# Kernel tuning notes

Hardware: AMD Instinct MI355X
Metric: run time of the kernel (lower is better)

The kernel has to match this reference:

```python
import jax, jax.numpy as jnp
import numpy as np

# SAWB clip coefficients (statistics-aware weight binning): alpha = C1*sqrt(E[w^2]) + C2*E[|w|]
SAWB_C1 = 12.68
SAWB_C2 = -12.80
Q_LEVELS = 127.0  # symmetric 8-bit


def sawb_quantize_sparse(W, mask):
    """Quantize only the nonzero (masked) weight values per-tensor, SAWB clip.
    Returns dequantized sparse weight (zeros stay zero), matching the
    original module which stores nnz values + indices and quantizes the
    nnz value vector."""
    m = mask.astype(W.dtype)
    n = jnp.maximum(jnp.sum(m), 1.0)
    m1 = jnp.sum(jnp.abs(W) * m) / n          # E[|w|] over nonzeros
    m2 = jnp.sum((W * W) * m) / n             # E[w^2] over nonzeros
    alpha = SAWB_C1 * jnp.sqrt(m2) + SAWB_C2 * m1
    scale = alpha / Q_LEVELS
    q = jnp.round(jnp.clip(W / scale, -Q_LEVELS, Q_LEVELS))
    return (q * scale) * m


def setup_inputs() -> dict:
    key = jax.random.key(0)
    k1, k2, k3, k4 = jax.random.split(key, 4)
    B, IC, H, Wsp = 16, 64, 224, 224
    OC, K = 64, 3
    x = jax.random.normal(k1, (B, IC, H, Wsp), dtype=jnp.float32)
    W = jax.random.normal(k2, (OC, IC, K, K), dtype=jnp.float32) * 0.05
    mask = jax.random.uniform(k3, (OC, IC, K, K)) > 0.9
    bias = jax.random.normal(k4, (OC,), dtype=jnp.float32) * 0.01
    return {"x": x, "W": W, "mask": mask, "bias": bias}


def reference(x, W, mask, bias):
    # Dequantized sparse weight (equivalent math to gather-based sparse
    # quantized conv kernel with fused dequant)
    Wq = sawb_quantize_sparse(W, mask)
    y = jax.lax.conv_general_dilated(
        x, Wq,
        window_strides=(1, 1),
        padding=((1, 1), (1, 1)),
        dimension_numbers=("NCHW", "OIHW", "NCHW"),
    )
    return y + bias[None, :, None, None]
```

## Files before the change

### kernel.cpp

```cpp
#include <hip/hip_runtime.h>
#include <hip/hip_bf16.h>
#include <math.h>

typedef __bf16 bfx8 __attribute__((ext_vector_type(8)));
typedef float f32x4 __attribute__((ext_vector_type(4)));

#define NELEM_W 36864
#define CHW     50176

__device__ __forceinline__ int detect_mask_kind(const void* mask, int tid, int nthreads,
                                                int* s_flags, int* s_kind) {
  if (tid < 8) s_flags[tid] = 0;
  __syncthreads();
  const unsigned int* mw = (const unsigned int*)mask;
  int lowbf = 0, notf32 = 0, anyf32 = 0, noti32 = 0, anyi1 = 0;
  for (int i = tid; i < 1024; i += nthreads) {
    unsigned v = mw[i];
    if ((v & 0xFFFFu) == 0x3F80u) lowbf = 1;
    if (!(v == 0u || v == 0x3F800000u)) notf32 = 1;
    if (v == 0x3F800000u) anyf32 = 1;
    if (!(v == 0u || v == 1u)) noti32 = 1;
    if (v == 1u) anyi1 = 1;
  }
  if (lowbf)  atomicOr(&s_flags[0], 1);
  if (notf32) atomicOr(&s_flags[1], 1);
  if (anyf32) atomicOr(&s_flags[2], 1);
  if (noti32) atomicOr(&s_flags[3], 1);
  if (anyi1)  atomicOr(&s_flags[4], 1);
  __syncthreads();
  if (tid == 0) {
    int kind;
    if (s_flags[0]) kind = 3;
    else if (!s_flags[1] && s_flags[2]) kind = 2;
    else if (!s_flags[3] && s_flags[4]) kind = 1;
    else kind = 0;
    *s_kind = kind;
  }
  __syncthreads();
  return *s_kind;
}

__device__ __forceinline__ bool mask_val(const void* mask, int kind, int e) {
  switch (kind) {
    case 1:  return ((const int*)mask)[e] != 0;
    case 2:  return ((const float*)mask)[e] != 0.0f;
    case 3:  return ((const unsigned short*)mask)[e] != 0;
    default: return ((const unsigned char*)mask)[e] != 0;
  }
}

__global__ __launch_bounds__(512) void stats_kernel(const float* __restrict__ W,
                                                    const void* __restrict__ mask,
                                                    float* __restrict__ ws_part) {
  __shared__ int s_flags[8]; __shared__ int s_kind;
  __shared__ float s_red[3][8];
  const int tid = threadIdx.x;
  int kind = detect_mask_kind(mask, tid, 512, s_flags, &s_kind);
  int e = blockIdx.x * 512 + tid;
  float w = W[e];
  bool m = mask_val(mask, kind, e);
  float s1 = m ? fabsf(w) : 0.f;
  float s2 = m ? w * w   : 0.f;
  float c  = m ? 1.f     : 0.f;
  #pragma unroll
  for (int o = 32; o > 0; o >>= 1) {
    s1 += __shfl_down(s1, o); s2 += __shfl_down(s2, o); c += __shfl_down(c, o);
  }
  int wv = tid >> 6;
  if ((tid & 63) == 0) { s_red[0][wv] = s1; s_red[1][wv] = s2; s_red[2][wv] = c; }
  __syncthreads();
  if (tid == 0) {
    float a = 0, b = 0, cc = 0;
    for (int i = 0; i < 8; i++) { a += s_red[0][i]; b += s_red[1][i]; cc += s_red[2][i]; }
    ws_part[blockIdx.x * 4 + 0] = a;
    ws_part[blockIdx.x * 4 + 1] = b;
    ws_part[blockIdx.x * 4 + 2] = cc;
  }
}

__global__ __launch_bounds__(512) void quant_kernel(const float* __restrict__ W,
                                                    const void* __restrict__ mask,
                                                    const float* __restrict__ ws_part,
                                                    float* __restrict__ ws_scale,
                                                    unsigned short* __restrict__ Bq) {
  __shared__ int s_flags[8]; __shared__ int s_kind;
  __shared__ float s_scale;
  const int tid = threadIdx.x;
  int kind = detect_mask_kind(mask, tid, 512, s_flags, &s_kind);
  if (tid == 0) {
    float a = 0, b = 0, cc = 0;
    for (int i = 0; i < 72; i++) { a += ws_part[i*4]; b += ws_part[i*4+1]; cc += ws_part[i*4+2]; }
    float n  = fmaxf(cc, 1.f);
    float m1 = a / n, m2 = b / n;
    float alpha = 12.68f * sqrtf(m2) - 12.80f * m1;
    float scale = alpha / 127.0f;
    s_scale = scale;
    if (blockIdx.x == 0) ws_scale[0] = scale;
  }
  __syncthreads();
  float scale = s_scale;
  int e = blockIdx.x * 512 + tid;
  float w = W[e];
  float q = 0.f;
  if (mask_val(mask, kind, e)) {
    float v = w / scale;
    v = fminf(fmaxf(v, -127.f), 127.f);
    q = rintf(v);
  }
  int kxy = e % 9; int t = e / 9; int ic = t & 63; int oc = t >> 6;
  __bf16 qb = (__bf16)q;
  Bq[(kxy * 64 + oc) * 64 + ic] = *(unsigned short*)&qb;
}

template<int NMF>
__device__ __forceinline__ void mfma_compute(const unsigned char* __restrict__ smem,
    const unsigned short* __restrict__ Bq, const float* __restrict__ ws_scale,
    const float* __restrict__ bias, float* __restrict__ out,
    int b, int y0, int x0, int wrow, int oc0, int mf0, int l15, int lg)
{
  f32x4 acc[NMF][2];
  #pragma unroll
  for (int m = 0; m < NMF; m++) { acc[m][0] = {0.f,0.f,0.f,0.f}; acc[m][1] = {0.f,0.f,0.f,0.f}; }

  #pragma unroll
  for (int ky = 0; ky < 3; ky++) {
    const int lrow = wrow + ky;
    #pragma unroll
    for (int kx = 0; kx < 3; kx++) {
      #pragma unroll
      for (int icb = 0; icb < 2; icb++) {
        const int ick = icb * 32 + lg * 8;
        const unsigned short* wp = Bq + (((ky*3 + kx) * 64 + oc0 + l15) * 64 + ick);
        bfx8 wf0 = *(const bfx8*)wp;
        bfx8 wf1 = *(const bfx8*)(wp + 16 * 64);
        #pragma unroll
        for (int m = 0; m < NMF; m++) {
          int colw = kx + (mf0 + m) * 16 + l15;
          int off  = ((lrow * 114 + colw) * 128 + ick * 2) ^ ((colw & 7) << 4);
          bfx8 xf  = *(const bfx8*)(smem + off);
          acc[m][0] = __builtin_amdgcn_mfma_f32_16x16x32_bf16(wf0, xf, acc[m][0], 0, 0, 0);
          acc[m][1] = __builtin_amdgcn_mfma_f32_16x16x32_bf16(wf1, xf, acc[m][1], 0, 0, 0);
        }
      }
    }
  }
  const float scale = ws_scale[0];
  const int yr = y0 + wrow;
  #pragma unroll
  for (int m = 0; m < NMF; m++) {
    #pragma unroll
    for (int n = 0; n < 2; n++) {
      #pragma unroll
      for (int r = 0; r < 4; r++) {
        int oc = oc0 + n * 16 + lg * 4 + r;
        float* op = out + (((size_t)(b * 64 + oc)) * 224 + yr) * 224 + x0 + (mf0 + m) * 16 + l15;
        *op = acc[m][n][r] * scale + bias[oc];
      }
    }
  }
}

__global__ __launch_bounds__(512, 4) void conv_kernel(const float* __restrict__ x,
    const unsigned short* __restrict__ Bq, const float* __restrict__ ws_scale,
    const float* __restrict__ bias, float* __restrict__ out)
{
  __shared__ __align__(16) unsigned char smem[4 * 114 * 128];
  const int tid = threadIdx.x;
  const int x0 = blockIdx.x * 112;
  const int y0 = blockIdx.y * 2;
  const int b  = blockIdx.z;

  for (int e = tid; e < 4 * 8 * 114; e += 512) {
    int col = e % 114; int t = e / 114; int icg = t & 7; int row = t >> 3;
    int grow = y0 - 1 + row, gcol = x0 - 1 + col;
    bfx8 v;
    if ((unsigned)grow < 224u && (unsigned)gcol < 224u) {
      const float* src = x + (((size_t)(b * 64 + icg * 8)) * 224 + grow) * 224 + gcol;
      #pragma unroll
      for (int j = 0; j < 8; j++) v[j] = (__bf16)src[j * CHW];
    } else {
      #pragma unroll
      for (int j = 0; j < 8; j++) v[j] = (__bf16)0.f;
    }
    int off = ((row * 114 + col) * 128 + icg * 16) ^ ((col & 7) << 4);
    *(bfx8*)(smem + off) = v;
  }
  __syncthreads();

  const int w = tid >> 6, lane = tid & 63;
  const int l15 = lane & 15, lg = lane >> 4;
  const int wrow = w >> 2;
  const int woc  = (w >> 1) & 1;
  const int wmf  = w & 1;
  const int oc0  = woc * 32;
  if (wmf == 0) mfma_compute<4>(smem, Bq, ws_scale, bias, out, b, y0, x0, wrow, oc0, 0, l15, lg);
  else          mfma_compute<3>(smem, Bq, ws_scale, bias, out, b, y0, x0, wrow, oc0, 4, l15, lg);
}

extern "C" void kernel_launch(void* const* d_in, const int* in_sizes, int n_in,
                              void* d_out, int out_size, void* d_ws, size_t ws_size,
                              hipStream_t stream) {
  const float* x    = (const float*)d_in[0];
  const float* W    = (const float*)d_in[1];
  const void*  mask = d_in[2];
  const float* bias = (const float*)d_in[3];
  float* out = (float*)d_out;

  float*          ws_part  = (float*)d_ws;
  float*          ws_scale = (float*)((char*)d_ws + 2048);
  unsigned short* Bq       = (unsigned short*)((char*)d_ws + 4096);

  stats_kernel<<<72, 512, 0, stream>>>(W, mask, ws_part);
  quant_kernel<<<72, 512, 0, stream>>>(W, mask, ws_part, ws_scale, Bq);
  dim3 grid(2, 112, 16);
  conv_kernel<<<grid, 512, 0, stream>>>(x, Bq, ws_scale, bias, out);
}
```

Baseline: 503.9 us.

## Retile conv to 4x64 output blocks with XCD-aware block remap

Changes each conv block's output tile from 2 rows by 112 columns to 4 rows by 64 columns. The input halo rows drop from 4 per 2 output rows to 6 per 4, which reduces redundant global loads and bf16 conversion. Every wave now handles a uniform 4 M-fragments across 4 rows by 2 OC halves, removing the 4/3 imbalance. Blocks are remapped so consecutive logical tiles interleave across the 8 XCDs, and the launch-bounds occupancy hint rises to 6. The cost is wasted compute in the last column tile (224 is not a multiple of 64), which is masked at the store.

```diff
diff --git a/kernel.cpp b/kernel.cpp
--- a/kernel.cpp
+++ b/kernel.cpp
@@ -112,15 +112,47 @@
   Bq[(kxy * 64 + oc) * 64 + ic] = *(unsigned short*)&qb;
 }
 
-template<int NMF>
-__device__ __forceinline__ void mfma_compute(const unsigned char* __restrict__ smem,
+__global__ __launch_bounds__(512, 6) void conv_kernel(const float* __restrict__ x,
     const unsigned short* __restrict__ Bq, const float* __restrict__ ws_scale,
-    const float* __restrict__ bias, float* __restrict__ out,
-    int b, int y0, int x0, int wrow, int oc0, int mf0, int l15, int lg)
+    const float* __restrict__ bias, float* __restrict__ out)
 {
-  f32x4 acc[NMF][2];
-  #pragma unroll
-  for (int m = 0; m < NMF; m++) { acc[m][0] = {0.f,0.f,0.f,0.f}; acc[m][1] = {0.f,0.f,0.f,0.f}; }
+  __shared__ __align__(16) unsigned char smem[6 * 66 * 128];
+  const int tid = threadIdx.x;
+
+  int lin = blockIdx.x + (int)(gridDim.x * (blockIdx.y + gridDim.y * blockIdx.z));
+  int logical = (lin & 7) * 448 + (lin >> 3);
+  const int bx = logical & 3;
+  int rr = logical >> 2;
+  const int by = rr % 56;
+  const int b  = rr / 56;
+  const int x0 = bx * 64;
+  const int y0 = by * 4;
+
+  for (int e = tid; e < 6 * 8 * 66; e += 512) {
+    int col = e % 66; int t = e / 66; int icg = t & 7; int row = t >> 3;
+    int grow = y0 - 1 + row, gcol = x0 - 1 + col;
+    bfx8 v;
+    if ((unsigned)grow < 224u && (unsigned)gcol < 224u) {
+      const float* src = x + (((size_t)(b * 64 + icg * 8)) * 224 + grow) * 224 + gcol;
+      #pragma unroll
+      for (int j = 0; j < 8; j++) v[j] = (__bf16)src[j * CHW];
+    } else {
+      #pragma unroll
+      for (int j = 0; j < 8; j++) v[j] = (__bf16)0.f;
+    }
+    int off = ((row * 66 + col) * 128 + icg * 16) ^ ((col & 7) << 4);
+    *(bfx8*)(smem + off) = v;
+  }
+  __syncthreads();
+
+  const int w = tid >> 6, lane = tid & 63;
+  const int l15 = lane & 15, lg = lane >> 4;
+  const int wrow = w >> 1;
+  const int oc0  = (w & 1) * 32;
+
+  f32x4 acc[4][2];
+  #pragma unroll
+  for (int m = 0; m < 4; m++) { acc[m][0] = {0.f,0.f,0.f,0.f}; acc[m][1] = {0.f,0.f,0.f,0.f}; }
 
   #pragma unroll
   for (int ky = 0; ky < 3; ky++) {
@@ -134,9 +166,9 @@
         bfx8 wf0 = *(const bfx8*)wp;
         bfx8 wf1 = *(const bfx8*)(wp + 16 * 64);
         #pragma unroll
-        for (int m = 0; m < NMF; m++) {
-          int colw = kx + (mf0 + m) * 16 + l15;
-          int off  = ((lrow * 114 + colw) * 128 + ick * 2) ^ ((colw & 7) << 4);
+        for (int m = 0; m < 4; m++) {
+          int colw = kx + m * 16 + l15;
+          int off  = ((lrow * 66 + colw) * 128 + ick * 2) ^ ((colw & 7) << 4);
           bfx8 xf  = *(const bfx8*)(smem + off);
           acc[m][0] = __builtin_amdgcn_mfma_f32_16x16x32_bf16(wf0, xf, acc[m][0], 0, 0, 0);
           acc[m][1] = __builtin_amdgcn_mfma_f32_16x16x32_bf16(wf1, xf, acc[m][1], 0, 0, 0);
@@ -144,57 +176,23 @@
       }
     }
   }
+
   const float scale = ws_scale[0];
   const int yr = y0 + wrow;
   #pragma unroll
-  for (int m = 0; m < NMF; m++) {
-    #pragma unroll
-    for (int n = 0; n < 2; n++) {
-      #pragma unroll
-      for (int r = 0; r < 4; r++) {
-        int oc = oc0 + n * 16 + lg * 4 + r;
-        float* op = out + (((size_t)(b * 64 + oc)) * 224 + yr) * 224 + x0 + (mf0 + m) * 16 + l15;
-        *op = acc[m][n][r] * scale + bias[oc];
+  for (int m = 0; m < 4; m++) {
+    const int gcol = x0 + m * 16 + l15;
+    if (gcol < 224) {
+      #pragma unroll
+      for (int n = 0; n < 2; n++) {
+        #pragma unroll
+        for (int r = 0; r < 4; r++) {
+          int oc = oc0 + n * 16 + lg * 4 + r;
+          out[(((size_t)(b * 64 + oc)) * 224 + yr) * 224 + gcol] = acc[m][n][r] * scale + bias[oc];
+        }
       }
     }
   }
-}
-
-__global__ __launch_bounds__(512, 4) void conv_kernel(const float* __restrict__ x,
-    const unsigned short* __restrict__ Bq, const float* __restrict__ ws_scale,
-    const float* __restrict__ bias, float* __restrict__ out)
-{
-  __shared__ __align__(16) unsigned char smem[4 * 114 * 128];
-  const int tid = threadIdx.x;
-  const int x0 = blockIdx.x * 112;
-  const int y0 = blockIdx.y * 2;
-  const int b  = blockIdx.z;
-
-  for (int e = tid; e < 4 * 8 * 114; e += 512) {
-    int col = e % 114; int t = e / 114; int icg = t & 7; int row = t >> 3;
-    int grow = y0 - 1 + row, gcol = x0 - 1 + col;
-    bfx8 v;
-    if ((unsigned)grow < 224u && (unsigned)gcol < 224u) {
-      const float* src = x + (((size_t)(b * 64 + icg * 8)) * 224 + grow) * 224 + gcol;
-      #pragma unroll
-      for (int j = 0; j < 8; j++) v[j] = (__bf16)src[j * CHW];
-    } else {
-      #pragma unroll
-      for (int j = 0; j < 8; j++) v[j] = (__bf16)0.f;
-    }
-    int off = ((row * 114 + col) * 128 + icg * 16) ^ ((col & 7) << 4);
-    *(bfx8*)(smem + off) = v;
-  }
-  __syncthreads();
-
-  const int w = tid >> 6, lane = tid & 63;
-  const int l15 = lane & 15, lg = lane >> 4;
-  const int wrow = w >> 2;
-  const int woc  = (w >> 1) & 1;
-  const int wmf  = w & 1;
-  const int oc0  = woc * 32;
-  if (wmf == 0) mfma_compute<4>(smem, Bq, ws_scale, bias, out, b, y0, x0, wrow, oc0, 0, l15, lg);
-  else          mfma_compute<3>(smem, Bq, ws_scale, bias, out, b, y0, x0, wrow, oc0, 4, l15, lg);
 }
 
 extern "C" void kernel_launch(void* const* d_in, const int* in_sizes, int n_in,
@@ -212,6 +210,6 @@
 
   stats_kernel<<<72, 512, 0, stream>>>(W, mask, ws_part);
   quant_kernel<<<72, 512, 0, stream>>>(W, mask, ws_part, ws_scale, Bq);
-  dim3 grid(2, 112, 16);
+  dim3 grid(4, 56, 16);
   conv_kernel<<<grid, 512, 0, stream>>>(x, Bq, ws_scale, bias, out);
 }
```

Measured after the change: 475.9 us. 1.06x faster.
